# Kernel tuning notes

Hardware: AMD Instinct MI355X
Metric: run time of the kernel (lower is better)

## Reference

```python
import jax, jax.numpy as jnp
import numpy as np

T = 128          # timesteps
N_NODES = 32
E = 512          # edges per timestep
IN_C = 64
HID = 128
SEQ_LEN = 16
OUT_C = (4, 2)
Y_DIM = 4


def setup_inputs() -> dict:
    key = jax.random.key(0)
    ks = jax.random.split(key, 16)
    s = 0.05
    f = jnp.float32
    inp = {
        'x': jax.random.normal(ks[0], (T, N_NODES, IN_C), f),
        'edge_index': jax.random.randint(ks[1], (T, 2, E), 0, N_NODES),
        'masks': jnp.ones((T, N_NODES), dtype=bool),
        'y': jax.random.normal(ks[2], (T, N_NODES, Y_DIM), f),
        'W1': jax.random.normal(ks[3], (IN_C, HID), f) * s,
        'b1': jnp.zeros((HID,), f),
        'W2': jax.random.normal(ks[4], (HID, HID), f) * s,
        'b2': jnp.zeros((HID,), f),
        # per-node LSTM layer 1 (torch gate order i,f,g,o)
        'Wih1': jax.random.normal(ks[5], (N_NODES, 4 * HID, HID), f) * s,
        'Whh1': jax.random.normal(ks[6], (N_NODES, 4 * HID, HID), f) * s,
        'bih1': jnp.zeros((N_NODES, 4 * HID), f),
        'bhh1': jnp.zeros((N_NODES, 4 * HID), f),
        # per-node LSTM layer 2
        'Wih2': jax.random.normal(ks[7], (N_NODES, 4 * HID, HID), f) * s,
        'Whh2': jax.random.normal(ks[8], (N_NODES, 4 * HID, HID), f) * s,
        'bih2': jnp.zeros((N_NODES, 4 * HID), f),
        'bhh2': jnp.zeros((N_NODES, 4 * HID), f),
        # per-node fc hidden->hidden
        'Wfc': jax.random.normal(ks[9], (N_NODES, HID, HID), f) * s,
        'bfc': jnp.zeros((N_NODES, HID), f),
        # per-node output heads
        'Wout0': jax.random.normal(ks[10], (N_NODES, OUT_C[0], HID), f) * s,
        'bout0': jnp.zeros((N_NODES, OUT_C[0]), f),
        'Wout1': jax.random.normal(ks[11], (N_NODES, OUT_C[1], HID), f) * s,
        'bout1': jnp.zeros((N_NODES, OUT_C[1]), f),
    }
    return inp


def _gcn(x_t, ei_t, W, b):
    # PyG GCNConv: add self-loops, symmetric normalization, out[col] += norm * (xW)[row]
    n = x_t.shape[0]
    loop = jnp.arange(n)
    row = jnp.concatenate([ei_t[0], loop])
    col = jnp.concatenate([ei_t[1], loop])
    deg = jax.ops.segment_sum(jnp.ones_like(col, dtype=x_t.dtype), col, num_segments=n)
    dinv = jnp.where(deg > 0, deg ** -0.5, 0.0)
    norm = dinv[row] * dinv[col]
    h = x_t @ W
    return jax.ops.segment_sum(norm[:, None] * h[row], col, num_segments=n) + b


def _lstm(seq, Wih, Whh, bih, bhh):
    # seq: [B, L, H]; torch LSTM, gates (i,f,g,o)
    xg = jnp.einsum('blh,gh->blg', seq, Wih) + bih + bhh    # [B,L,4H]
    xg = jnp.swapaxes(xg, 0, 1)                              # [L,B,4H]
    B, H = seq.shape[0], Whh.shape[1]
    def step(carry, g_x):
        h, c = carry
        g = g_x + h @ Whh.T
        i, fgt, gg, o = jnp.split(g, 4, axis=-1)
        c = jax.nn.sigmoid(fgt) * c + jax.nn.sigmoid(i) * jnp.tanh(gg)
        h = jax.nn.sigmoid(o) * jnp.tanh(c)
        return (h, c), h
    h0 = jnp.zeros((B, H), seq.dtype)
    _, hs = jax.lax.scan(step, (h0, h0), xg)
    return jnp.swapaxes(hs, 0, 1)                            # [B,L,H]


def reference(x, edge_index, masks, y, W1, b1, W2, b2,
              Wih1, Whh1, bih1, bhh1, Wih2, Whh2, bih2, bhh2,
              Wfc, bfc, Wout0, bout0, Wout1, bout1):
    # per-timestep 2-layer GCN with relu (dropout is identity in eval mode)
    def gcn_pair(xt, et):
        h = jax.nn.relu(_gcn(xt, et, W1, b1))
        return jax.nn.relu(_gcn(h, et, W2, b2))
    h = jax.vmap(gcn_pair)(x, edge_index)                    # [T,N,H]

    # generate_sequences_node: sliding windows of length SEQ_LEN over masked
    # event features, zero-padded at the front. masks are all-ones here so
    # events == timesteps and max_events == T (static shapes for jit).
    idx = jnp.arange(T)[:, None] - (SEQ_LEN - 1) + jnp.arange(SEQ_LEN)[None, :]  # [T,L]
    valid = (idx >= 0).astype(h.dtype)
    seqs = h[jnp.clip(idx, 0)] * valid[:, :, None, None]     # [T,L,N,H]
    seqs = jnp.transpose(seqs, (2, 0, 1, 3))                 # [N,T,L,H]

    o = jax.vmap(_lstm)(seqs, Wih1, Whh1, bih1, bhh1)        # per-node weights
    o = jax.vmap(_lstm)(o, Wih2, Whh2, bih2, bhh2)
    last = jax.nn.relu(o)[:, :, -1, :]                        # [N,T,H] (fc then [:, -1] == [:, -1] then fc)
    fc = jnp.einsum('nbh,nkh->nbk', last, Wfc) + bfc[:, None, :]
    o0 = jnp.einsum('nbh,nkh->nbk', fc, Wout0) + bout0[:, None, :]
    o1 = jnp.einsum('nbh,nkh->nbk', fc, Wout1) + bout1[:, None, :]
    out0 = jnp.transpose(o0, (1, 0, 2))                       # [max_events,N,out_c0]
    out1 = jnp.transpose(o1, (1, 0, 2))                       # [max_events,N,out_c1]
    # filtered targets: y[:, i, :][mask_i] padded to max_events; identity for all-ones mask
    targets = y
    return (out0, out1, targets)
```

## Files before the change

kernel.cpp:

```cpp
#include <hip/hip_runtime.h>


#define T_STEPS 128
#define HID     128
#define G4      512
#define SEQ     16

typedef unsigned short u16;
typedef unsigned int   u32;
typedef __attribute__((ext_vector_type(8))) short bf16x8;
typedef __attribute__((ext_vector_type(4))) float f32x4;
typedef __attribute__((ext_vector_type(4))) u16   u16x4;

__device__ __forceinline__ float bf2f(u16 u) {
  union { u32 i; float f; } v; v.i = ((u32)u) << 16; return v.f;
}
__device__ __forceinline__ u16 f2bf(float f) {
  union { u32 i; float f; } v; v.f = f;
  const u32 i = v.i;
  return (u16)((i + 0x7fffu + ((i >> 16) & 1u)) >> 16);
}
__device__ __forceinline__ float sigm(float x) {
  return __builtin_amdgcn_rcpf(1.f + __expf(-x));
}
__device__ __forceinline__ float tanh_fast(float x) {
  return 1.f - 2.f * __builtin_amdgcn_rcpf(1.f + __expf(2.f * x));
}
__device__ __forceinline__ float clampg(float x) { return fminf(fmaxf(x, -25.f), 25.f); }

__device__ __forceinline__ float ldf(const void* p, size_t i, int isbf) {
  return isbf ? bf2f(((const u16*)p)[i]) : ((const float*)p)[i];
}
__device__ __forceinline__ bf16x8 ld8(const void* p, size_t o, int isbf) {
  if (isbf) return *(const bf16x8*)((const u16*)p + o);
  const float* f = (const float*)p + o;
  bf16x8 r;
  #pragma unroll
  for (int j = 0; j < 8; ++j) r[j] = (short)f2bf(f[j]);
  return r;
}
__device__ __forceinline__ int lde(const int* ei, int idx, int i64) {
  return i64 ? ei[idx * 2] : ei[idx];
}

__global__ __launch_bounds__(512) void gcn_kernel(
    const void* __restrict__ x, const int* __restrict__ ei,
    const void* __restrict__ W1, const void* __restrict__ b1,
    const void* __restrict__ W2, const void* __restrict__ b2,
    u32* __restrict__ flags, u16* __restrict__ Hb)
{
  const int t = blockIdx.x;
  const int tid = threadIdx.x;
  const int wave = tid >> 6, lane = tid & 63;
  const int quad = lane >> 4, l16 = lane & 15;

  __shared__ u16 sXA[32 * 72];
  __shared__ u16 sW1T[128 * 72];
  __shared__ u16 sW2T[128 * 136];
  __shared__ u16 sAmB[32 * 40];
  __shared__ float sAm[32 * 33];
  __shared__ u16 sT[128 * 40];
  __shared__ u16 sHA[32 * 136];
  __shared__ int sdeg[32];
  __shared__ float sdinv[32];
  __shared__ int dc1, dc2;

  if (tid == 0) { dc1 = 0; dc2 = 0; }
  __syncthreads();
  if (tid < 256) {
    const u32 w = ((const u32*)x)[tid];
    const u16 lo = (u16)(w & 0xffffu);
    const float a = fabsf(bf2f(lo));
    if (lo != 0 && a >= 9.5e-7f && a <= 8.f) atomicAdd(&dc1, 1);
    if (ei[2 * tid + 1] != 0) atomicAdd(&dc2, 1);
  }
  __syncthreads();
  const int isbf = (dc1 >= 128) ? 1 : 0;
  const int i64  = (dc2 < 8) ? 1 : 0;
  if (t == 0 && tid == 0) { flags[0] = (u32)isbf; flags[1] = (u32)i64; }

  for (int idx = tid; idx < 2048; idx += 512) {
    const int m = idx >> 6, k = idx & 63;
    sXA[m * 72 + k] = f2bf(ldf(x, (size_t)t * 2048 + idx, isbf));
  }
  for (int idx = tid; idx < 8192; idx += 512) {
    const int k = idx >> 7, nn = idx & 127;
    sW1T[nn * 72 + k] = f2bf(ldf(W1, idx, isbf));
  }
  for (int idx = tid; idx < 16384; idx += 512) {
    const int k = idx >> 7, nn = idx & 127;
    sW2T[nn * 136 + k] = f2bf(ldf(W2, idx, isbf));
  }
  for (int i = tid; i < 32 * 33; i += 512) sAm[i] = 0.f;
  if (tid < 32) sdeg[tid] = 0;
  __syncthreads();
  if (tid < 512) {
    const int cd = lde(ei, t * 1024 + 512 + tid, i64);
    if ((u32)cd < 32u) atomicAdd(&sdeg[cd], 1);
  }
  __syncthreads();
  if (tid < 32) sdinv[tid] = rsqrtf((float)(sdeg[tid] + 1));
  __syncthreads();
  if (tid < 512) {
    const int r  = lde(ei, t * 1024 + tid, i64);
    const int cd = lde(ei, t * 1024 + 512 + tid, i64);
    if ((u32)r < 32u && (u32)cd < 32u)
      atomicAdd(&sAm[cd * 33 + r], sdinv[r] * sdinv[cd]);
  }
  if (tid < 32) atomicAdd(&sAm[tid * 33 + tid], sdinv[tid] * sdinv[tid]);
  __syncthreads();

  for (int idx = tid; idx < 1024; idx += 512) {
    const int m = idx >> 5, k = idx & 31;
    sAmB[m * 40 + k] = f2bf(sAm[m * 33 + k]);
  }
  {
    const int nc = wave * 16 + l16;
    f32x4 c0 = {0.f,0.f,0.f,0.f}, c1 = {0.f,0.f,0.f,0.f};
    #pragma unroll
    for (int kc = 0; kc < 2; ++kc) {
      const bf16x8 a0 = *(const bf16x8*)&sXA[l16 * 72 + kc * 32 + quad * 8];
      const bf16x8 a1 = *(const bf16x8*)&sXA[(16 + l16) * 72 + kc * 32 + quad * 8];
      const bf16x8 bb = *(const bf16x8*)&sW1T[nc * 72 + kc * 32 + quad * 8];
      c0 = __builtin_amdgcn_mfma_f32_16x16x32_bf16(a0, bb, c0, 0, 0, 0);
      c1 = __builtin_amdgcn_mfma_f32_16x16x32_bf16(a1, bb, c1, 0, 0, 0);
    }
    #pragma unroll
    for (int r = 0; r < 4; ++r) {
      sT[nc * 40 + quad * 4 + r]      = f2bf(c0[r]);
      sT[nc * 40 + 16 + quad * 4 + r] = f2bf(c1[r]);
    }
  }
  __syncthreads();
  {
    const int nc = wave * 16 + l16;
    const bf16x8 a0 = *(const bf16x8*)&sAmB[l16 * 40 + quad * 8];
    const bf16x8 a1 = *(const bf16x8*)&sAmB[(16 + l16) * 40 + quad * 8];
    const bf16x8 bb = *(const bf16x8*)&sT[nc * 40 + quad * 8];
    f32x4 c0 = {0.f,0.f,0.f,0.f}, c1 = {0.f,0.f,0.f,0.f};
    c0 = __builtin_amdgcn_mfma_f32_16x16x32_bf16(a0, bb, c0, 0, 0, 0);
    c1 = __builtin_amdgcn_mfma_f32_16x16x32_bf16(a1, bb, c1, 0, 0, 0);
    const float bv = ldf(b1, nc, isbf);
    #pragma unroll
    for (int r = 0; r < 4; ++r) {
      float v0 = c0[r] + bv, v1 = c1[r] + bv;
      sHA[(quad * 4 + r) * 136 + nc]      = f2bf(v0 > 0.f ? v0 : 0.f);
      sHA[(16 + quad * 4 + r) * 136 + nc] = f2bf(v1 > 0.f ? v1 : 0.f);
    }
  }
  __syncthreads();
  {
    const int nc = wave * 16 + l16;
    f32x4 c0 = {0.f,0.f,0.f,0.f}, c1 = {0.f,0.f,0.f,0.f};
    #pragma unroll
    for (int kc = 0; kc < 4; ++kc) {
      const bf16x8 a0 = *(const bf16x8*)&sHA[l16 * 136 + kc * 32 + quad * 8];
      const bf16x8 a1 = *(const bf16x8*)&sHA[(16 + l16) * 136 + kc * 32 + quad * 8];
      const bf16x8 bb = *(const bf16x8*)&sW2T[nc * 136 + kc * 32 + quad * 8];
      c0 = __builtin_amdgcn_mfma_f32_16x16x32_bf16(a0, bb, c0, 0, 0, 0);
      c1 = __builtin_amdgcn_mfma_f32_16x16x32_bf16(a1, bb, c1, 0, 0, 0);
    }
    #pragma unroll
    for (int r = 0; r < 4; ++r) {
      sT[nc * 40 + quad * 4 + r]      = f2bf(c0[r]);
      sT[nc * 40 + 16 + quad * 4 + r] = f2bf(c1[r]);
    }
  }
  __syncthreads();
  {
    const int nc = wave * 16 + l16;
    const bf16x8 a0 = *(const bf16x8*)&sAmB[l16 * 40 + quad * 8];
    const bf16x8 a1 = *(const bf16x8*)&sAmB[(16 + l16) * 40 + quad * 8];
    const bf16x8 bb = *(const bf16x8*)&sT[nc * 40 + quad * 8];
    f32x4 c0 = {0.f,0.f,0.f,0.f}, c1 = {0.f,0.f,0.f,0.f};
    c0 = __builtin_amdgcn_mfma_f32_16x16x32_bf16(a0, bb, c0, 0, 0, 0);
    c1 = __builtin_amdgcn_mfma_f32_16x16x32_bf16(a1, bb, c1, 0, 0, 0);
    const float bv = ldf(b2, nc, isbf);
    #pragma unroll
    for (int r = 0; r < 4; ++r) {
      float v0 = c0[r] + bv, v1 = c1[r] + bv;
      Hb[((size_t)t * 32 + quad * 4 + r) * 128 + nc]      = f2bf(v0 > 0.f ? v0 : 0.f);
      Hb[((size_t)t * 32 + 16 + quad * 4 + r) * 128 + nc] = f2bf(v1 > 0.f ? v1 : 0.f);
    }
  }
}

__global__ __launch_bounds__(512) void lstm_kernel(
    const void* __restrict__ Wih1, const void* __restrict__ Whh1,
    const void* __restrict__ Wih2, const void* __restrict__ Whh2,
    const void* __restrict__ bih1, const void* __restrict__ bhh1,
    const void* __restrict__ bih2, const void* __restrict__ bhh2,
    const u16* __restrict__ Hb, const u32* __restrict__ flags,
    u16* __restrict__ HLAST)
{
  const int isbf = (int)flags[0];
  const int b = blockIdx.x;
  const int n = b & 31, wg = b >> 5;
  const int t0 = wg * 16;
  const int tid = threadIdx.x;
  const int wave = tid >> 6, lane = tid & 63;
  const int quad = lane >> 4, l16 = lane & 15;
  const int col = wave * 16 + l16;

  __shared__ __align__(16) char arena[131072];
  __shared__ __align__(16) u16 sH[2][16 * 136];
  u16* sHB  = (u16*)arena;
  u16* xg1L = (u16*)(arena + 8704);
  u16* h1sL = (u16*)(arena + 41472);

  const size_t Wbase = (size_t)n * (G4 * HID);

  for (int idx = tid; idx < 32 * 128; idx += 512) {
    const int row = idx >> 7, cc = idx & 127;
    const int tp = t0 - 15 + row;
    sHB[row * 136 + cc] =
        (tp >= 0 && tp < T_STEPS) ? Hb[((size_t)tp * 32 + n) * 128 + cc] : (u16)0;
  }
  float bbv[4];
  #pragma unroll
  for (int t = 0; t < 4; ++t)
    bbv[t] = ldf(bih1, n * 512 + t * 128 + col, isbf) +
             ldf(bhh1, n * 512 + t * 128 + col, isbf);
  __syncthreads();
  {
    u16 pk[2][4][4];
    #pragma unroll
    for (int t = 0; t < 4; ++t) {
      const size_t gb = Wbase + (size_t)(t * 128 + col) * HID;
      f32x4 a0 = {0.f,0.f,0.f,0.f}, a1 = {0.f,0.f,0.f,0.f};
      #pragma unroll
      for (int kc = 0; kc < 4; ++kc) {
        const bf16x8 wf = ld8(Wih1, gb + kc * 32 + quad * 8, isbf);
        const bf16x8 h0 = *(const bf16x8*)&sHB[l16 * 136 + kc * 32 + quad * 8];
        const bf16x8 h1v = *(const bf16x8*)&sHB[(16 + l16) * 136 + kc * 32 + quad * 8];
        a0 = __builtin_amdgcn_mfma_f32_16x16x32_bf16(h0, wf, a0, 0, 0, 0);
        a1 = __builtin_amdgcn_mfma_f32_16x16x32_bf16(h1v, wf, a1, 0, 0, 0);
      }
      #pragma unroll
      for (int r = 0; r < 4; ++r) {
        pk[0][r][t] = f2bf(a0[r] + bbv[t]);
        pk[1][r][t] = f2bf(a1[r] + bbv[t]);
      }
    }
    #pragma unroll
    for (int g2 = 0; g2 < 2; ++g2)
      #pragma unroll
      for (int r = 0; r < 4; ++r) {
        u16x4 v = {pk[g2][r][0], pk[g2][r][1], pk[g2][r][2], pk[g2][r][3]};
        *(u16x4*)&xg1L[((size_t)(g2 * 16 + quad * 4 + r) * 128 + col) * 4] = v;
      }
  }

  bf16x8 bfr1[4][4];
  #pragma unroll
  for (int t = 0; t < 4; ++t) {
    const size_t gb = Wbase + (size_t)(t * 128 + col) * HID;
    #pragma unroll
    for (int kc = 0; kc < 4; ++kc)
      bfr1[t][kc] = ld8(Whh1, gb + kc * 32 + quad * 8, isbf);
  }
  #pragma unroll
  for (int t = 0; t < 4; ++t)
    #pragma unroll
    for (int kc = 0; kc < 4; ++kc)
      asm volatile("" : "+a"(bfr1[t][kc]));

  float c1v[4] = {0.f, 0.f, 0.f, 0.f};
  __syncthreads();

  for (int l = 0; l < SEQ; ++l) {
    f32x4 acc[4];
    #pragma unroll
    for (int t = 0; t < 4; ++t) { acc[t][0]=0.f; acc[t][1]=0.f; acc[t][2]=0.f; acc[t][3]=0.f; }
    if (l) {
      bf16x8 af[4];
      #pragma unroll
      for (int kc = 0; kc < 4; ++kc)
        af[kc] = *(const bf16x8*)&h1sL[(l - 1) * 2176 + l16 * 136 + kc * 32 + quad * 8];
      #pragma unroll
      for (int t = 0; t < 4; ++t)
        #pragma unroll
        for (int kc = 0; kc < 4; ++kc)
          acc[t] = __builtin_amdgcn_mfma_f32_16x16x32_bf16(af[kc], bfr1[t][kc], acc[t], 0, 0, 0);
    }
    #pragma unroll
    for (int r = 0; r < 4; ++r) {
      const int row = quad * 4 + r + l;
      const u16x4 gv = *(const u16x4*)&xg1L[((size_t)row * 128 + col) * 4];
      const float gi = clampg(acc[0][r] + bf2f(gv[0]));
      const float gf = clampg(acc[1][r] + bf2f(gv[1]));
      const float gg = clampg(acc[2][r] + bf2f(gv[2]));
      const float go = clampg(acc[3][r] + bf2f(gv[3]));
      c1v[r] = sigm(gf) * c1v[r] + sigm(gi) * tanh_fast(gg);
      h1sL[l * 2176 + (quad * 4 + r) * 136 + col] = f2bf(sigm(go) * tanh_fast(c1v[r]));
    }
    __syncthreads();
  }

  bf16x8 bfri[4][4], bfrh[4][4];
  #pragma unroll
  for (int t = 0; t < 4; ++t) {
    const size_t gb = Wbase + (size_t)(t * 128 + col) * HID;
    #pragma unroll
    for (int kc = 0; kc < 4; ++kc) {
      bfri[t][kc] = ld8(Wih2, gb + kc * 32 + quad * 8, isbf);
      bfrh[t][kc] = ld8(Whh2, gb + kc * 32 + quad * 8, isbf);
    }
  }
  #pragma unroll
  for (int t = 0; t < 4; ++t)
    #pragma unroll
    for (int kc = 0; kc < 4; ++kc) {
      asm volatile("" : "+a"(bfri[t][kc]));
      asm volatile("" : "+a"(bfrh[t][kc]));
    }

  float bias2[4];
  #pragma unroll
  for (int t = 0; t < 4; ++t)
    bias2[t] = ldf(bih2, n * 512 + t * 128 + col, isbf) +
               ldf(bhh2, n * 512 + t * 128 + col, isbf);

  float c2v[4] = {0.f, 0.f, 0.f, 0.f};
  int p = 0;
  for (int s = 0; s < SEQ; ++s) {
    bf16x8 af[4];
    #pragma unroll
    for (int kc = 0; kc < 4; ++kc)
      af[kc] = *(const bf16x8*)&h1sL[s * 2176 + l16 * 136 + kc * 32 + quad * 8];
    f32x4 acc[4];
    #pragma unroll
    for (int t = 0; t < 4; ++t) { acc[t][0]=0.f; acc[t][1]=0.f; acc[t][2]=0.f; acc[t][3]=0.f; }
    #pragma unroll
    for (int t = 0; t < 4; ++t)
      #pragma unroll
      for (int kc = 0; kc < 4; ++kc)
        acc[t] = __builtin_amdgcn_mfma_f32_16x16x32_bf16(af[kc], bfri[t][kc], acc[t], 0, 0, 0);
    if (s) {
      bf16x8 ah[4];
      #pragma unroll
      for (int kc = 0; kc < 4; ++kc)
        ah[kc] = *(const bf16x8*)&sH[p][l16 * 136 + kc * 32 + quad * 8];
      #pragma unroll
      for (int t = 0; t < 4; ++t)
        #pragma unroll
        for (int kc = 0; kc < 4; ++kc)
          acc[t] = __builtin_amdgcn_mfma_f32_16x16x32_bf16(ah[kc], bfrh[t][kc], acc[t], 0, 0, 0);
    }
    u16 hv[4];
    #pragma unroll
    for (int r = 0; r < 4; ++r) {
      const float gi = clampg(acc[0][r] + bias2[0]);
      const float gf = clampg(acc[1][r] + bias2[1]);
      const float gg = clampg(acc[2][r] + bias2[2]);
      const float go = clampg(acc[3][r] + bias2[3]);
      c2v[r] = sigm(gf) * c2v[r] + sigm(gi) * tanh_fast(gg);
      hv[r] = f2bf(sigm(go) * tanh_fast(c2v[r]));
    }
    #pragma unroll
    for (int r = 0; r < 4; ++r) {
      sH[1 - p][(quad * 4 + r) * 136 + col] = hv[r];
      if (s == SEQ - 1)
        HLAST[((size_t)n * T_STEPS + t0 + quad * 4 + r) * HID + col] = hv[r];
    }
    __syncthreads();
    p ^= 1;
  }
}

__global__ __launch_bounds__(256) void head_kernel(
    const u16* __restrict__ HLAST, const void* __restrict__ Wfc, const void* __restrict__ bfc,
    const void* __restrict__ Wout0, const void* __restrict__ bout0,
    const void* __restrict__ Wout1, const void* __restrict__ bout1,
    const void* __restrict__ y, const u32* __restrict__ flags,
    float* __restrict__ out)
{
  const int isbf = (int)flags[0];
  const int b = blockIdx.x;
  const int n = b >> 2, tc = (b & 3) * 32;
  const int tid = threadIdx.x;
  const int wave = tid >> 6, lane = tid & 63;
  const int quad = lane >> 4, l16 = lane & 15;

  __shared__ u16 sLA[32 * 136];
  __shared__ float sF[32 * 132];

  for (int i = tid; i < 32 * 128; i += 256) {
    const int r = i >> 7, cc = i & 127;
    const u16 hv = HLAST[((size_t)n * T_STEPS + tc + r) * 128 + cc];
    const float v = bf2f(hv);
    sLA[r * 136 + cc] = v > 0.f ? hv : (u16)0;
  }
  __syncthreads();

  {
    f32x4 acc[2][2];
    #pragma unroll
    for (int mt = 0; mt < 2; ++mt)
      #pragma unroll
      for (int nt = 0; nt < 2; ++nt) { acc[mt][nt][0]=0.f; acc[mt][nt][1]=0.f; acc[mt][nt][2]=0.f; acc[mt][nt][3]=0.f; }
    #pragma unroll
    for (int kc = 0; kc < 4; ++kc) {
      const bf16x8 a0 = *(const bf16x8*)&sLA[l16 * 136 + kc * 32 + quad * 8];
      const bf16x8 a1 = *(const bf16x8*)&sLA[(16 + l16) * 136 + kc * 32 + quad * 8];
      #pragma unroll
      for (int nt = 0; nt < 2; ++nt) {
        const int col = wave * 32 + nt * 16 + l16;
        const bf16x8 bb = ld8(Wfc, (size_t)n * 16384 + (size_t)col * 128 + kc * 32 + quad * 8, isbf);
        acc[0][nt] = __builtin_amdgcn_mfma_f32_16x16x32_bf16(a0, bb, acc[0][nt], 0, 0, 0);
        acc[1][nt] = __builtin_amdgcn_mfma_f32_16x16x32_bf16(a1, bb, acc[1][nt], 0, 0, 0);
      }
    }
    #pragma unroll
    for (int nt = 0; nt < 2; ++nt) {
      const int col = wave * 32 + nt * 16 + l16;
      const float bv = ldf(bfc, n * 128 + col, isbf);
      #pragma unroll
      for (int r = 0; r < 4; ++r) {
        sF[(quad * 4 + r) * 132 + col]      = acc[0][nt][r] + bv;
        sF[(16 + quad * 4 + r) * 132 + col] = acc[1][nt][r] + bv;
      }
    }
  }
  __syncthreads();

  if (tid < 192) {
    const int tt = tid / 6, o = tid % 6;
    size_t wb; float a;
    if (o < 4) { wb = ((size_t)n * 4 + o) * 128;       a = ldf(bout0, n * 4 + o, isbf); }
    else       { wb = ((size_t)n * 2 + (o - 4)) * 128; a = ldf(bout1, n * 2 + o - 4, isbf); }
    for (int k = 0; k < 128; ++k)
      a += sF[tt * 132 + k] * (o < 4 ? ldf(Wout0, wb + k, isbf) : ldf(Wout1, wb + k, isbf));
    const int t = tc + tt;
    if (o < 4) out[((size_t)t * 32 + n) * 4 + o] = a;
    else       out[16384 + ((size_t)t * 32 + n) * 2 + (o - 4)] = a;
  }

  if (tid < 128) {
    const int tt = tid >> 2, k = tid & 3;
    const int t = tc + tt;
    const size_t i = ((size_t)t * 32 + n) * 4 + k;
    out[24576 + i] = ldf(y, i, isbf);
  }
}

extern "C" void kernel_launch(void* const* d_in, const int* in_sizes, int n_in,
                              void* d_out, int out_size, void* d_ws, size_t ws_size,
                              hipStream_t stream)
{
  (void)out_size;
  static const int DICT_M[22]  = {262144,131072,4096,16384,8192,128,16384,128,
                                  2097152,2097152,16384,16384,2097152,2097152,
                                  16384,16384,524288,4096,16384,128,8192,64};
  static const int DICT_NM[21] = {262144,131072,16384,8192,128,16384,128,
                                  2097152,2097152,16384,16384,2097152,2097152,
                                  16384,16384,524288,4096,16384,128,8192,64};
  static const int SORT_M[22]  = {8192,16384,524288,2097152,2097152,2097152,
                                  2097152,16384,8192,128,128,4096,16384,16384,
                                  16384,16384,128,64,131072,4096,262144,16384};
  static const int SORT_NM[21] = {8192,16384,524288,2097152,2097152,2097152,
                                  2097152,16384,8192,128,128,4096,16384,16384,
                                  16384,16384,128,64,131072,262144,16384};
  auto matches = [&](const int* exp, int cnt, int ei_idx) -> bool {
    if (n_in != cnt) return false;
    for (int i = 0; i < cnt; ++i) {
      if (i == ei_idx) {
        if (in_sizes[i] != 131072 && in_sizes[i] != 262144) return false;
      } else if (in_sizes[i] != exp[i]) return false;
    }
    return true;
  };
  int map[21];
  auto set_dict = [&](int sh) {
    map[0] = 0; map[1] = 1;
    for (int s = 2; s < 21; ++s) map[s] = s + 1 + sh;
  };
  auto set_sorted = [&](int xi) {
    map[0] = xi; map[1] = 18; map[2] = xi + 1;
    map[3] = 0;  map[4] = 9;  map[5] = 1;  map[6] = 10;
    map[7] = 5;  map[8] = 3;  map[9] = 14; map[10] = 12;
    map[11] = 6; map[12] = 4; map[13] = 15; map[14] = 13;
    map[15] = 2; map[16] = 11; map[17] = 7; map[18] = 16;
    map[19] = 8; map[20] = 17;
  };
  if      (matches(DICT_M, 22, 1))  set_dict(0);
  else if (matches(DICT_NM, 21, 1)) set_dict(-1);
  else if (matches(SORT_M, 22, 18)) set_sorted(20);
  else if (matches(SORT_NM, 21, 18)) set_sorted(19);
  else set_dict((n_in >= 22) ? 0 : -1);

  const void* x     = d_in[map[0]];
  const int*  ei    = (const int*)d_in[map[1]];
  const void* y     = d_in[map[2]];
  const void* W1    = d_in[map[3]];
  const void* b1    = d_in[map[4]];
  const void* W2    = d_in[map[5]];
  const void* b2    = d_in[map[6]];
  const void* Wih1  = d_in[map[7]];
  const void* Whh1  = d_in[map[8]];
  const void* bih1  = d_in[map[9]];
  const void* bhh1  = d_in[map[10]];
  const void* Wih2  = d_in[map[11]];
  const void* Whh2  = d_in[map[12]];
  const void* bih2  = d_in[map[13]];
  const void* bhh2  = d_in[map[14]];
  const void* Wfc   = d_in[map[15]];
  const void* bfc   = d_in[map[16]];
  const void* Wout0 = d_in[map[17]];
  const void* bout0 = d_in[map[18]];
  const void* Wout1 = d_in[map[19]];
  const void* bout1 = d_in[map[20]];
  float* out = (float*)d_out;

  const size_t WS_NEED = 4096 + 1048576 + 1048576;
  if (ws_size < WS_NEED) return;
  char* ws = (char*)d_ws;
  u32* flags  = (u32*)ws;
  u16* Hb     = (u16*)(ws + 4096);
  u16* HLAST  = (u16*)(ws + 4096 + 1048576);

  gcn_kernel <<<dim3(128), dim3(512), 0, stream>>>(x, ei, W1, b1, W2, b2, flags, Hb);
  lstm_kernel<<<dim3(256), dim3(512), 0, stream>>>(Wih1, Whh1, Wih2, Whh2,
                                                   bih1, bhh1, bih2, bhh2,
                                                   Hb, flags, HLAST);
  head_kernel<<<dim3(128), dim3(256), 0, stream>>>(HLAST, Wfc, bfc, Wout0, bout0,
                                                   Wout1, bout1, y, flags, out);
}
```

Baseline: 222.1 us.

## Wavefront-interleave the two LSTM layers in one loop with Whh1 staged in LDS

The two stacked LSTM recurrences now run in a single skewed loop. Each iteration computes layer-1 step i and layer-2 step i-1, which halves the number of serial barrier-separated steps and gives the MFMA units independent work to overlap. To make room, the layer-1 recurrent weights move from AGPR registers into a swizzled 128KB LDS buffer. The layer-1 input-gate precompute spills to a global workspace scratch buffer, and small double-buffered rings replace the per-step h1 history. The cost is LDS bandwidth for the Whh1 operands, global traffic for the gate scratch, and LDS use that allows only one block per CU.

After: 223.0 us. About the same (+0.4%).

```diff
diff --git a/kernel.cpp b/kernel.cpp
--- a/kernel.cpp
+++ b/kernel.cpp
@@ -191,7 +191,7 @@
     const void* __restrict__ bih1, const void* __restrict__ bhh1,
     const void* __restrict__ bih2, const void* __restrict__ bhh2,
     const u16* __restrict__ Hb, const u32* __restrict__ flags,
-    u16* __restrict__ HLAST)
+    u16* __restrict__ XG1, u16* __restrict__ HLAST)
 {
   const int isbf = (int)flags[0];
   const int b = blockIdx.x;
@@ -202,12 +202,12 @@
   const int quad = lane >> 4, l16 = lane & 15;
   const int col = wave * 16 + l16;
 
-  __shared__ __align__(16) char arena[131072];
-  __shared__ __align__(16) u16 sH[2][16 * 136];
-  u16* sHB  = (u16*)arena;
-  u16* xg1L = (u16*)(arena + 8704);
-  u16* h1sL = (u16*)(arena + 41472);
-
+  __shared__ __align__(16) u16 sW[512 * 128];
+  __shared__ __align__(16) u16 ring1[2][16 * 136];
+  __shared__ __align__(16) u16 ring2[2][16 * 136];
+  u16* sHB = (u16*)ring1;
+
+  u16* xg1 = XG1 + (size_t)b * (32 * 512);
   const size_t Wbase = (size_t)n * (G4 * HID);
 
   for (int idx = tid; idx < 32 * 128; idx += 512) {
@@ -216,12 +216,20 @@
     sHB[row * 136 + cc] =
         (tp >= 0 && tp < T_STEPS) ? Hb[((size_t)tp * 32 + n) * 128 + cc] : (u16)0;
   }
+  {
+    const int g = tid;
+    const size_t gb = Wbase + (size_t)g * HID;
+    #pragma unroll
+    for (int c = 0; c < 16; ++c)
+      *(bf16x8*)&sW[g * 128 + ((c ^ (g & 15)) * 8)] = ld8(Whh1, gb + c * 8, isbf);
+  }
   float bbv[4];
   #pragma unroll
   for (int t = 0; t < 4; ++t)
     bbv[t] = ldf(bih1, n * 512 + t * 128 + col, isbf) +
              ldf(bhh1, n * 512 + t * 128 + col, isbf);
   __syncthreads();
+
   {
     u16 pk[2][4][4];
     #pragma unroll
@@ -247,54 +255,8 @@
       #pragma unroll
       for (int r = 0; r < 4; ++r) {
         u16x4 v = {pk[g2][r][0], pk[g2][r][1], pk[g2][r][2], pk[g2][r][3]};
-        *(u16x4*)&xg1L[((size_t)(g2 * 16 + quad * 4 + r) * 128 + col) * 4] = v;
-      }
-  }
-
-  bf16x8 bfr1[4][4];
-  #pragma unroll
-  for (int t = 0; t < 4; ++t) {
-    const size_t gb = Wbase + (size_t)(t * 128 + col) * HID;
-    #pragma unroll
-    for (int kc = 0; kc < 4; ++kc)
-      bfr1[t][kc] = ld8(Whh1, gb + kc * 32 + quad * 8, isbf);
-  }
-  #pragma unroll
-  for (int t = 0; t < 4; ++t)
-    #pragma unroll
-    for (int kc = 0; kc < 4; ++kc)
-      asm volatile("" : "+a"(bfr1[t][kc]));
-
-  float c1v[4] = {0.f, 0.f, 0.f, 0.f};
-  __syncthreads();
-
-  for (int l = 0; l < SEQ; ++l) {
-    f32x4 acc[4];
-    #pragma unroll
-    for (int t = 0; t < 4; ++t) { acc[t][0]=0.f; acc[t][1]=0.f; acc[t][2]=0.f; acc[t][3]=0.f; }
-    if (l) {
-      bf16x8 af[4];
-      #pragma unroll
-      for (int kc = 0; kc < 4; ++kc)
-        af[kc] = *(const bf16x8*)&h1sL[(l - 1) * 2176 + l16 * 136 + kc * 32 + quad * 8];
-      #pragma unroll
-      for (int t = 0; t < 4; ++t)
-        #pragma unroll
-        for (int kc = 0; kc < 4; ++kc)
-          acc[t] = __builtin_amdgcn_mfma_f32_16x16x32_bf16(af[kc], bfr1[t][kc], acc[t], 0, 0, 0);
-    }
-    #pragma unroll
-    for (int r = 0; r < 4; ++r) {
-      const int row = quad * 4 + r + l;
-      const u16x4 gv = *(const u16x4*)&xg1L[((size_t)row * 128 + col) * 4];
-      const float gi = clampg(acc[0][r] + bf2f(gv[0]));
-      const float gf = clampg(acc[1][r] + bf2f(gv[1]));
-      const float gg = clampg(acc[2][r] + bf2f(gv[2]));
-      const float go = clampg(acc[3][r] + bf2f(gv[3]));
-      c1v[r] = sigm(gf) * c1v[r] + sigm(gi) * tanh_fast(gg);
-      h1sL[l * 2176 + (quad * 4 + r) * 136 + col] = f2bf(sigm(go) * tanh_fast(c1v[r]));
-    }
-    __syncthreads();
+        *(u16x4*)&xg1[((size_t)(g2 * 16 + quad * 4 + r) * 128 + col) * 4] = v;
+      }
   }
 
   bf16x8 bfri[4][4], bfrh[4][4];
@@ -314,57 +276,107 @@
       asm volatile("" : "+a"(bfri[t][kc]));
       asm volatile("" : "+a"(bfrh[t][kc]));
     }
-
   float bias2[4];
   #pragma unroll
   for (int t = 0; t < 4; ++t)
     bias2[t] = ldf(bih2, n * 512 + t * 128 + col, isbf) +
                ldf(bhh2, n * 512 + t * 128 + col, isbf);
 
+  float c1v[4] = {0.f, 0.f, 0.f, 0.f};
   float c2v[4] = {0.f, 0.f, 0.f, 0.f};
-  int p = 0;
-  for (int s = 0; s < SEQ; ++s) {
+  __syncthreads();
+
+  for (int i = 0; i <= SEQ; ++i) {
+    const bool doB = (i < SEQ);
+    const bool doD = (i >= 1);
+
+    u16x4 gvb[4];
+    if (doB) {
+      #pragma unroll
+      for (int r = 0; r < 4; ++r)
+        gvb[r] = *(const u16x4*)&xg1[((size_t)(quad * 4 + r + i) * 128 + col) * 4];
+    }
     bf16x8 af[4];
-    #pragma unroll
-    for (int kc = 0; kc < 4; ++kc)
-      af[kc] = *(const bf16x8*)&h1sL[s * 2176 + l16 * 136 + kc * 32 + quad * 8];
-    f32x4 acc[4];
-    #pragma unroll
-    for (int t = 0; t < 4; ++t) { acc[t][0]=0.f; acc[t][1]=0.f; acc[t][2]=0.f; acc[t][3]=0.f; }
-    #pragma unroll
-    for (int t = 0; t < 4; ++t)
+    if (i > 0) {
       #pragma unroll
       for (int kc = 0; kc < 4; ++kc)
-        acc[t] = __builtin_amdgcn_mfma_f32_16x16x32_bf16(af[kc], bfri[t][kc], acc[t], 0, 0, 0);
-    if (s) {
-      bf16x8 ah[4];
-      #pragma unroll
-      for (int kc = 0; kc < 4; ++kc)
-        ah[kc] = *(const bf16x8*)&sH[p][l16 * 136 + kc * 32 + quad * 8];
+        af[kc] = *(const bf16x8*)&ring1[(i - 1) & 1][l16 * 136 + kc * 32 + quad * 8];
+    }
+
+    f32x4 accB[4];
+    #pragma unroll
+    for (int t = 0; t < 4; ++t) { accB[t][0]=0.f; accB[t][1]=0.f; accB[t][2]=0.f; accB[t][3]=0.f; }
+    if (doB && i > 0) {
       #pragma unroll
       for (int t = 0; t < 4; ++t)
         #pragma unroll
         for (int kc = 0; kc < 4; ++kc)
-          acc[t] = __builtin_amdgcn_mfma_f32_16x16x32_bf16(ah[kc], bfrh[t][kc], acc[t], 0, 0, 0);
-    }
-    u16 hv[4];
-    #pragma unroll
-    for (int r = 0; r < 4; ++r) {
-      const float gi = clampg(acc[0][r] + bias2[0]);
-      const float gf = clampg(acc[1][r] + bias2[1]);
-      const float gg = clampg(acc[2][r] + bias2[2]);
-      const float go = clampg(acc[3][r] + bias2[3]);
-      c2v[r] = sigm(gf) * c2v[r] + sigm(gi) * tanh_fast(gg);
-      hv[r] = f2bf(sigm(go) * tanh_fast(c2v[r]));
-    }
-    #pragma unroll
-    for (int r = 0; r < 4; ++r) {
-      sH[1 - p][(quad * 4 + r) * 136 + col] = hv[r];
-      if (s == SEQ - 1)
-        HLAST[((size_t)n * T_STEPS + t0 + quad * 4 + r) * HID + col] = hv[r];
+          accB[t] = __builtin_amdgcn_mfma_f32_16x16x32_bf16(
+              af[kc], *(const bf16x8*)&sW[(t * 128 + col) * 128 + (((kc * 4 + quad) ^ l16) * 8)],
+              accB[t], 0, 0, 0);
+    }
+    f32x4 accD[4];
+    #pragma unroll
+    for (int t = 0; t < 4; ++t) { accD[t][0]=0.f; accD[t][1]=0.f; accD[t][2]=0.f; accD[t][3]=0.f; }
+    if (doD) {
+      #pragma unroll
+      for (int t = 0; t < 4; ++t)
+        #pragma unroll
+        for (int kc = 0; kc < 4; ++kc)
+          accD[t] = __builtin_amdgcn_mfma_f32_16x16x32_bf16(af[kc], bfri[t][kc], accD[t], 0, 0, 0);
+      if (i >= 2) {
+        bf16x8 ah[4];
+        #pragma unroll
+        for (int kc = 0; kc < 4; ++kc)
+          ah[kc] = *(const bf16x8*)&ring2[i & 1][l16 * 136 + kc * 32 + quad * 8];
+        #pragma unroll
+        for (int t = 0; t < 4; ++t)
+          #pragma unroll
+          for (int kc = 0; kc < 4; ++kc)
+            accD[t] = __builtin_amdgcn_mfma_f32_16x16x32_bf16(ah[kc], bfrh[t][kc], accD[t], 0, 0, 0);
+      }
+    }
+
+    u16 hv1[4], hv2[4];
+    if (doB) {
+      #pragma unroll
+      for (int r = 0; r < 4; ++r) {
+        const float gi = clampg(accB[0][r] + bf2f(gvb[r][0]));
+        const float gf = clampg(accB[1][r] + bf2f(gvb[r][1]));
+        const float gg = clampg(accB[2][r] + bf2f(gvb[r][2]));
+        const float go = clampg(accB[3][r] + bf2f(gvb[r][3]));
+        c1v[r] = sigm(gf) * c1v[r] + sigm(gi) * tanh_fast(gg);
+        hv1[r] = f2bf(sigm(go) * tanh_fast(c1v[r]));
+      }
+    }
+    if (doD) {
+      #pragma unroll
+      for (int r = 0; r < 4; ++r) {
+        const float gi = clampg(accD[0][r] + bias2[0]);
+        const float gf = clampg(accD[1][r] + bias2[1]);
+        const float gg = clampg(accD[2][r] + bias2[2]);
+        const float go = clampg(accD[3][r] + bias2[3]);
+        c2v[r] = sigm(gf) * c2v[r] + sigm(gi) * tanh_fast(gg);
+        hv2[r] = f2bf(sigm(go) * tanh_fast(c2v[r]));
+      }
+    }
+
+    if (doB) {
+      #pragma unroll
+      for (int r = 0; r < 4; ++r)
+        ring1[i & 1][(quad * 4 + r) * 136 + col] = hv1[r];
+    }
+    if (doD) {
+      #pragma unroll
+      for (int r = 0; r < 4; ++r)
+        ring2[(i - 1) & 1][(quad * 4 + r) * 136 + col] = hv2[r];
+      if (i - 1 == SEQ - 1) {
+        #pragma unroll
+        for (int r = 0; r < 4; ++r)
+          HLAST[((size_t)n * T_STEPS + t0 + quad * 4 + r) * HID + col] = hv2[r];
+      }
     }
     __syncthreads();
-    p ^= 1;
   }
 }
 
@@ -512,17 +524,21 @@
   const void* bout1 = d_in[map[20]];
   float* out = (float*)d_out;
 
-  const size_t WS_NEED = 4096 + 1048576 + 1048576;
+  const size_t OFF_HB  = 4096;
+  const size_t OFF_HL  = OFF_HB + 1048576;
+  const size_t OFF_XG1 = OFF_HL + 1048576;
+  const size_t WS_NEED = OFF_XG1 + 8388608;
   if (ws_size < WS_NEED) return;
   char* ws = (char*)d_ws;
   u32* flags  = (u32*)ws;
-  u16* Hb     = (u16*)(ws + 4096);
-  u16* HLAST  = (u16*)(ws + 4096 + 1048576);
+  u16* Hb     = (u16*)(ws + OFF_HB);
+  u16* HLAST  = (u16*)(ws + OFF_HL);
+  u16* XG1    = (u16*)(ws + OFF_XG1);
 
   gcn_kernel <<<dim3(128), dim3(512), 0, stream>>>(x, ei, W1, b1, W2, b2, flags, Hb);
   lstm_kernel<<<dim3(256), dim3(512), 0, stream>>>(Wih1, Whh1, Wih2, Whh2,
                                                    bih1, bhh1, bih2, bhh2,
-                                                   Hb, flags, HLAST);
+                                                   Hb, flags, XG1, HLAST);
   head_kernel<<<dim3(128), dim3(256), 0, stream>>>(HLAST, Wfc, bfc, Wout0, bout0,
                                                    Wout1, bout1, y, flags, out);
 }
```

## Fuse head into LSTM kernel, move y copy into GCN, vectorize bf16 loads

Applied to the files above, without the earlier changes.

Removes the separate head kernel. Each LSTM block now keeps its last hidden states in shared memory and computes the fc layer and both output heads itself, which removes one launch and the HLAST round trip through global memory. The y passthrough copy moves into the GCN kernel. The GCN input staging gets a bf16 fast path with vectorized x loads, and the output-head dot product reads weights eight at a time. The trade-off is extra tail work and shared-memory reuse (aliasing the arena) in the already heavy LSTM kernel.

After: 195.8 us. 11.8% less time.

```diff
diff --git a/kernel.cpp b/kernel.cpp
--- a/kernel.cpp
+++ b/kernel.cpp
@@ -47,7 +47,8 @@
     const void* __restrict__ x, const int* __restrict__ ei,
     const void* __restrict__ W1, const void* __restrict__ b1,
     const void* __restrict__ W2, const void* __restrict__ b2,
-    u32* __restrict__ flags, u16* __restrict__ Hb)
+    const void* __restrict__ y, u32* __restrict__ flags,
+    u16* __restrict__ Hb, float* __restrict__ out)
 {
   const int t = blockIdx.x;
   const int tid = threadIdx.x;
@@ -79,17 +80,37 @@
   const int i64  = (dc2 < 8) ? 1 : 0;
   if (t == 0 && tid == 0) { flags[0] = (u32)isbf; flags[1] = (u32)i64; }
 
-  for (int idx = tid; idx < 2048; idx += 512) {
-    const int m = idx >> 6, k = idx & 63;
-    sXA[m * 72 + k] = f2bf(ldf(x, (size_t)t * 2048 + idx, isbf));
-  }
-  for (int idx = tid; idx < 8192; idx += 512) {
-    const int k = idx >> 7, nn = idx & 127;
-    sW1T[nn * 72 + k] = f2bf(ldf(W1, idx, isbf));
-  }
-  for (int idx = tid; idx < 16384; idx += 512) {
-    const int k = idx >> 7, nn = idx & 127;
-    sW2T[nn * 136 + k] = f2bf(ldf(W2, idx, isbf));
+  if (tid < 128) out[24576 + t * 128 + tid] = ldf(y, (size_t)t * 128 + tid, isbf);
+
+  if (isbf) {
+    const u16* xu  = (const u16*)x;
+    const u16* w1u = (const u16*)W1;
+    const u16* w2u = (const u16*)W2;
+    for (int v = tid; v < 256; v += 512) {
+      const int m = v >> 3, k8 = (v & 7) * 8;
+      *(bf16x8*)&sXA[m * 72 + k8] = *(const bf16x8*)&xu[(size_t)t * 2048 + m * 64 + k8];
+    }
+    for (int idx = tid; idx < 8192; idx += 512) {
+      const int k = idx >> 7, nn = idx & 127;
+      sW1T[nn * 72 + k] = w1u[idx];
+    }
+    for (int idx = tid; idx < 16384; idx += 512) {
+      const int k = idx >> 7, nn = idx & 127;
+      sW2T[nn * 136 + k] = w2u[idx];
+    }
+  } else {
+    for (int idx = tid; idx < 2048; idx += 512) {
+      const int m = idx >> 6, k = idx & 63;
+      sXA[m * 72 + k] = f2bf(ldf(x, (size_t)t * 2048 + idx, 0));
+    }
+    for (int idx = tid; idx < 8192; idx += 512) {
+      const int k = idx >> 7, nn = idx & 127;
+      sW1T[nn * 72 + k] = f2bf(ldf(W1, idx, 0));
+    }
+    for (int idx = tid; idx < 16384; idx += 512) {
+      const int k = idx >> 7, nn = idx & 127;
+      sW2T[nn * 136 + k] = f2bf(ldf(W2, idx, 0));
+    }
   }
   for (int i = tid; i < 32 * 33; i += 512) sAm[i] = 0.f;
   if (tid < 32) sdeg[tid] = 0;
@@ -191,7 +212,10 @@
     const void* __restrict__ bih1, const void* __restrict__ bhh1,
     const void* __restrict__ bih2, const void* __restrict__ bhh2,
     const u16* __restrict__ Hb, const u32* __restrict__ flags,
-    u16* __restrict__ HLAST)
+    const void* __restrict__ Wfc, const void* __restrict__ bfc,
+    const void* __restrict__ Wout0, const void* __restrict__ bout0,
+    const void* __restrict__ Wout1, const void* __restrict__ bout1,
+    float* __restrict__ out)
 {
   const int isbf = (int)flags[0];
   const int b = blockIdx.x;
@@ -204,9 +228,11 @@
 
   __shared__ __align__(16) char arena[131072];
   __shared__ __align__(16) u16 sH[2][16 * 136];
-  u16* sHB  = (u16*)arena;
-  u16* xg1L = (u16*)(arena + 8704);
-  u16* h1sL = (u16*)(arena + 41472);
+  u16*  sHB   = (u16*)arena;
+  u16*  sLast = (u16*)arena;
+  u16*  xg1L  = (u16*)(arena + 8704);
+  float* sF   = (float*)(arena + 8704);
+  u16*  h1sL  = (u16*)(arena + 41472);
 
   const size_t Wbase = (size_t)n * (G4 * HID);
 
@@ -361,86 +387,39 @@
     for (int r = 0; r < 4; ++r) {
       sH[1 - p][(quad * 4 + r) * 136 + col] = hv[r];
       if (s == SEQ - 1)
-        HLAST[((size_t)n * T_STEPS + t0 + quad * 4 + r) * HID + col] = hv[r];
+        sLast[(quad * 4 + r) * 136 + col] = (hv[r] & 0x8000u) ? (u16)0 : hv[r];
     }
     __syncthreads();
     p ^= 1;
   }
-}
-
-__global__ __launch_bounds__(256) void head_kernel(
-    const u16* __restrict__ HLAST, const void* __restrict__ Wfc, const void* __restrict__ bfc,
-    const void* __restrict__ Wout0, const void* __restrict__ bout0,
-    const void* __restrict__ Wout1, const void* __restrict__ bout1,
-    const void* __restrict__ y, const u32* __restrict__ flags,
-    float* __restrict__ out)
-{
-  const int isbf = (int)flags[0];
-  const int b = blockIdx.x;
-  const int n = b >> 2, tc = (b & 3) * 32;
-  const int tid = threadIdx.x;
-  const int wave = tid >> 6, lane = tid & 63;
-  const int quad = lane >> 4, l16 = lane & 15;
-
-  __shared__ u16 sLA[32 * 136];
-  __shared__ float sF[32 * 132];
-
-  for (int i = tid; i < 32 * 128; i += 256) {
-    const int r = i >> 7, cc = i & 127;
-    const u16 hv = HLAST[((size_t)n * T_STEPS + tc + r) * 128 + cc];
-    const float v = bf2f(hv);
-    sLA[r * 136 + cc] = v > 0.f ? hv : (u16)0;
-  }
-  __syncthreads();
 
   {
-    f32x4 acc[2][2];
-    #pragma unroll
-    for (int mt = 0; mt < 2; ++mt)
-      #pragma unroll
-      for (int nt = 0; nt < 2; ++nt) { acc[mt][nt][0]=0.f; acc[mt][nt][1]=0.f; acc[mt][nt][2]=0.f; acc[mt][nt][3]=0.f; }
+    f32x4 acc = {0.f, 0.f, 0.f, 0.f};
     #pragma unroll
     for (int kc = 0; kc < 4; ++kc) {
-      const bf16x8 a0 = *(const bf16x8*)&sLA[l16 * 136 + kc * 32 + quad * 8];
-      const bf16x8 a1 = *(const bf16x8*)&sLA[(16 + l16) * 136 + kc * 32 + quad * 8];
-      #pragma unroll
-      for (int nt = 0; nt < 2; ++nt) {
-        const int col = wave * 32 + nt * 16 + l16;
-        const bf16x8 bb = ld8(Wfc, (size_t)n * 16384 + (size_t)col * 128 + kc * 32 + quad * 8, isbf);
-        acc[0][nt] = __builtin_amdgcn_mfma_f32_16x16x32_bf16(a0, bb, acc[0][nt], 0, 0, 0);
-        acc[1][nt] = __builtin_amdgcn_mfma_f32_16x16x32_bf16(a1, bb, acc[1][nt], 0, 0, 0);
-      }
-    }
-    #pragma unroll
-    for (int nt = 0; nt < 2; ++nt) {
-      const int col = wave * 32 + nt * 16 + l16;
-      const float bv = ldf(bfc, n * 128 + col, isbf);
-      #pragma unroll
-      for (int r = 0; r < 4; ++r) {
-        sF[(quad * 4 + r) * 132 + col]      = acc[0][nt][r] + bv;
-        sF[(16 + quad * 4 + r) * 132 + col] = acc[1][nt][r] + bv;
-      }
-    }
-  }
-  __syncthreads();
-
-  if (tid < 192) {
+      const bf16x8 a  = *(const bf16x8*)&sLast[l16 * 136 + kc * 32 + quad * 8];
+      const bf16x8 bb = ld8(Wfc, (size_t)n * 16384 + (size_t)col * 128 + kc * 32 + quad * 8, isbf);
+      acc = __builtin_amdgcn_mfma_f32_16x16x32_bf16(a, bb, acc, 0, 0, 0);
+    }
+    const float bv = ldf(bfc, n * 128 + col, isbf);
+    #pragma unroll
+    for (int r = 0; r < 4; ++r)
+      sF[(quad * 4 + r) * 132 + col] = acc[r] + bv;
+  }
+  __syncthreads();
+  if (tid < 96) {
     const int tt = tid / 6, o = tid % 6;
     size_t wb; float a;
     if (o < 4) { wb = ((size_t)n * 4 + o) * 128;       a = ldf(bout0, n * 4 + o, isbf); }
     else       { wb = ((size_t)n * 2 + (o - 4)) * 128; a = ldf(bout1, n * 2 + o - 4, isbf); }
-    for (int k = 0; k < 128; ++k)
-      a += sF[tt * 132 + k] * (o < 4 ? ldf(Wout0, wb + k, isbf) : ldf(Wout1, wb + k, isbf));
-    const int t = tc + tt;
+    for (int k8 = 0; k8 < 16; ++k8) {
+      const bf16x8 wv = ld8(o < 4 ? Wout0 : Wout1, wb + k8 * 8, isbf);
+      #pragma unroll
+      for (int j = 0; j < 8; ++j) a += sF[tt * 132 + k8 * 8 + j] * bf2f((u16)wv[j]);
+    }
+    const int t = t0 + tt;
     if (o < 4) out[((size_t)t * 32 + n) * 4 + o] = a;
     else       out[16384 + ((size_t)t * 32 + n) * 2 + (o - 4)] = a;
-  }
-
-  if (tid < 128) {
-    const int tt = tid >> 2, k = tid & 3;
-    const int t = tc + tt;
-    const size_t i = ((size_t)t * 32 + n) * 4 + k;
-    out[24576 + i] = ldf(y, i, isbf);
   }
 }
 
@@ -512,17 +491,16 @@
   const void* bout1 = d_in[map[20]];
   float* out = (float*)d_out;
 
-  const size_t WS_NEED = 4096 + 1048576 + 1048576;
+  const size_t WS_NEED = 4096 + 1048576;
   if (ws_size < WS_NEED) return;
   char* ws = (char*)d_ws;
   u32* flags  = (u32*)ws;
   u16* Hb     = (u16*)(ws + 4096);
-  u16* HLAST  = (u16*)(ws + 4096 + 1048576);
-
-  gcn_kernel <<<dim3(128), dim3(512), 0, stream>>>(x, ei, W1, b1, W2, b2, flags, Hb);
+
+  gcn_kernel <<<dim3(128), dim3(512), 0, stream>>>(x, ei, W1, b1, W2, b2, y, flags, Hb, out);
   lstm_kernel<<<dim3(256), dim3(512), 0, stream>>>(Wih1, Whh1, Wih2, Whh2,
                                                    bih1, bhh1, bih2, bhh2,
-                                                   Hb, flags, HLAST);
-  head_kernel<<<dim3(128), dim3(256), 0, stream>>>(HLAST, Wfc, bfc, Wout0, bout0,
-                                                   Wout1, bout1, y, flags, out);
-}
+                                                   Hb, flags,
+                                                   Wfc, bfc, Wout0, bout0, Wout1, bout1,
+                                                   out);
+}
```
